# Performance work log

Hardware: AMD Instinct MI355X
Metric: run time of the kernel (lower is better)

The kernel has to match this reference:

```python
import jax, jax.numpy as jnp
import numpy as np

N, NUM_MEM, HIDDEN = 131072, 1024, 256
TEMPERATURE = 0.5
EPS = 1e-12  # matches F.normalize default eps


def setup_inputs() -> dict:
    key = jax.random.key(0)
    k1, k2 = jax.random.split(key)
    x = jax.random.normal(k1, (N, HIDDEN), dtype=jnp.float32)
    # xavier_uniform-style init for the memory bank
    limit = float(np.sqrt(6.0 / (NUM_MEM + HIDDEN)))
    memories = jax.random.uniform(k2, (NUM_MEM, HIDDEN), dtype=jnp.float32,
                                  minval=-limit, maxval=limit)
    return {"x": x, "memories": memories}


def reference(x, memories):
    # cosine similarity: normalize both sides, then QK^T
    x_norm = x / jnp.maximum(jnp.linalg.norm(x, axis=-1, keepdims=True), EPS)
    mem_norm = memories / jnp.maximum(
        jnp.linalg.norm(memories, axis=-1, keepdims=True), EPS)
    logits = jnp.einsum('nd,md->nm', x_norm, mem_norm) / TEMPERATURE
    weight = jax.nn.softmax(logits, axis=-1)        # [N, num_memories]
    read = jnp.einsum('nm,md->nd', weight, memories)  # weighted memory read
    return read
```

## Files before the change

### kernel.cpp

```cpp
#include <hip/hip_runtime.h>
#include <hip/hip_bf16.h>
#include <stdint.h>

#define HIDDEN 256
#define NMEM   1024
#define NTILES 32
#define LOG2E  1.44269504088896340736f

typedef __attribute__((ext_vector_type(8)))  short bf16x8;
typedef __attribute__((ext_vector_type(16))) float f32x16;
typedef unsigned short ushort_t;
typedef unsigned int   uint_t;

__device__ __forceinline__ ushort_t f2bf(float f) {
  uint_t u = __builtin_bit_cast(uint_t, f);
  u += 0x7FFFu + ((u >> 16) & 1u);
  return (ushort_t)(u >> 16);
}

__device__ __forceinline__ void gload_lds16(const void* g, void* l) {
  __builtin_amdgcn_global_load_lds(
      (const __attribute__((address_space(1))) uint_t*)g,
      (__attribute__((address_space(3))) uint_t*)l, 16, 0, 0);
}

__global__ void prep_kernel(const float* __restrict__ mem,
                            ushort_t* __restrict__ wsm,
                            ushort_t* __restrict__ wsv) {
  const int m = blockIdx.x;
  const int k = threadIdx.x;
  float v = mem[m * HIDDEN + k];
  float ss = v * v;
  #pragma unroll
  for (int off = 1; off < 64; off <<= 1) ss += __shfl_xor(ss, off);
  __shared__ float red[4];
  if ((k & 63) == 0) red[k >> 6] = ss;
  __syncthreads();
  const float tot = red[0] + red[1] + red[2] + red[3];
  const float inv = 1.0f / fmaxf(sqrtf(tot), 1e-12f);
  const ushort_t hn = f2bf(v * inv);
  const ushort_t hv = f2bf(v);
  const int t = m >> 5, mr = m & 31;
  wsm[t * 8192 + mr * 256 + (((k >> 3) ^ (mr & 7)) << 3) + (k & 7)] = hn;
  wsv[t * 8192 + k * 32  + (((mr >> 3) ^ ((k >> 1) & 3)) << 3) + (mr & 7)] = hv;
}

__global__ __launch_bounds__(256, 2) void mem_kernel(
    const float* __restrict__ x, const ushort_t* __restrict__ wsm,
    const ushort_t* __restrict__ wsv, float* __restrict__ out) {
  __shared__ __align__(16) char lds[65536];
  const int tid  = threadIdx.x;
  const int lane = tid & 63;
  const int wave = tid >> 6;
  const int col  = lane & 31;
  const int hi   = lane >> 5;
  const int row0 = blockIdx.x * 128 + wave * 32;
  const char* gm = (const char*)wsm;
  const char* gv = (const char*)wsv;

  auto stage = [&](int t, int buf) {
    const int bb = buf << 15;
    const int go = t * 16384;
    #pragma unroll
    for (int r = 0; r < 4; ++r) {
      const int o = wave * 4096 + r * 1024;
      gload_lds16(gm + go + o + lane * 16, lds + bb + o);
      gload_lds16(gv + go + o + lane * 16, lds + bb + 16384 + o);
    }
  };

  stage(0, 0);

  bf16x8 xb[16];
  float ss = 0.f;
  const float* xr = x + (size_t)(row0 + col) * HIDDEN + hi * 8;
  #pragma unroll
  for (int ks = 0; ks < 16; ++ks) {
    float4 a = *(const float4*)(xr + ks * 16);
    float4 b = *(const float4*)(xr + ks * 16 + 4);
    ss += a.x*a.x + a.y*a.y + a.z*a.z + a.w*a.w
        + b.x*b.x + b.y*b.y + b.z*b.z + b.w*b.w;
    xb[ks][0] = (short)f2bf(a.x); xb[ks][1] = (short)f2bf(a.y);
    xb[ks][2] = (short)f2bf(a.z); xb[ks][3] = (short)f2bf(a.w);
    xb[ks][4] = (short)f2bf(b.x); xb[ks][5] = (short)f2bf(b.y);
    xb[ks][6] = (short)f2bf(b.z); xb[ks][7] = (short)f2bf(b.w);
  }
  ss += __shfl_xor(ss, 32);
  const float myscale = (2.0f * LOG2E) / fmaxf(sqrtf(ss), 1e-12f);

  const f32x16 zz = {0.f,0.f,0.f,0.f, 0.f,0.f,0.f,0.f,
                     0.f,0.f,0.f,0.f, 0.f,0.f,0.f,0.f};
  f32x16 o8[8];
  #pragma unroll
  for (int i = 0; i < 8; ++i) o8[i] = zz;
  float den = 0.f;

  const int ck7 = col & 7;
  const int ck3 = (col >> 1) & 3;

  __syncthreads();

  for (int t = 0; t < NTILES; ++t) {
    const int mb = (t & 1) << 15;
    const int vb = mb + 16384;
    if (t < NTILES - 1) stage(t + 1, (t & 1) ^ 1);
    __builtin_amdgcn_s_setprio(1);

    const char* ab = lds + mb + col * 512;
    f32x16 s0 = zz, s1 = zz;
    #pragma unroll
    for (int ks2 = 0; ks2 < 8; ++ks2) {
      bf16x8 a0 = *(const bf16x8*)(ab + (((4*ks2 + hi)     ^ ck7) << 4));
      bf16x8 a1 = *(const bf16x8*)(ab + (((4*ks2 + 2 + hi) ^ ck7) << 4));
      s0 = __builtin_amdgcn_mfma_f32_32x32x16_bf16(a0, xb[2*ks2],   s0, 0,0,0);
      s1 = __builtin_amdgcn_mfma_f32_32x32x16_bf16(a1, xb[2*ks2+1], s1, 0,0,0);
    }

    float p[16];
    #pragma unroll
    for (int r = 0; r < 16; ++r) {
      const float pv = exp2f((s0[r] + s1[r]) * myscale);
      den += pv;
      p[r] = pv;
    }

    bf16x8 pa[2];
    #pragma unroll
    for (int ks = 0; ks < 2; ++ks) {
      const int b0 = ks * 8;
      uint_t w0 = (uint_t)f2bf(p[b0+0]) | ((uint_t)f2bf(p[b0+1]) << 16);
      uint_t w1 = (uint_t)f2bf(p[b0+2]) | ((uint_t)f2bf(p[b0+3]) << 16);
      uint_t w2 = (uint_t)f2bf(p[b0+4]) | ((uint_t)f2bf(p[b0+5]) << 16);
      uint_t w3 = (uint_t)f2bf(p[b0+6]) | ((uint_t)f2bf(p[b0+7]) << 16);
      asm("v_permlane32_swap_b32 %0, %1" : "+v"(w0), "+v"(w2));
      asm("v_permlane32_swap_b32 %0, %1" : "+v"(w1), "+v"(w3));
      uint4 u = {w0, w1, w2, w3};
      pa[ks] = __builtin_bit_cast(bf16x8, u);
    }

    const char* vrb = lds + vb + col * 64;
    #pragma unroll
    for (int ks = 0; ks < 2; ++ks) {
      const int cc = ((2*ks + hi) ^ ck3) << 4;
      #pragma unroll
      for (int d0 = 0; d0 < 8; ++d0) {
        bf16x8 vf = *(const bf16x8*)(vrb + d0 * 2048 + cc);
        o8[d0] = __builtin_amdgcn_mfma_f32_32x32x16_bf16(pa[ks], vf, o8[d0], 0,0,0);
      }
    }
    __builtin_amdgcn_s_setprio(0);
    __syncthreads();
  }

  den += __shfl_xor(den, 32);
  const float rden = 1.0f / den;
  float rdv[16];
  #pragma unroll
  for (int r = 0; r < 16; ++r)
    rdv[r] = __shfl(rden, (r & 3) + 8 * (r >> 2) + 4 * hi);

  float* op = out + (size_t)row0 * HIDDEN;
  #pragma unroll
  for (int d0 = 0; d0 < 8; ++d0) {
    #pragma unroll
    for (int r = 0; r < 16; ++r) {
      const int rw = (r & 3) + 8 * (r >> 2) + 4 * hi;
      op[(size_t)rw * HIDDEN + d0 * 32 + col] = o8[d0][r] * rdv[r];
    }
  }
}

extern "C" void kernel_launch(void* const* d_in, const int* in_sizes, int n_in,
                              void* d_out, int out_size, void* d_ws, size_t ws_size,
                              hipStream_t stream) {
  const float* x   = (const float*)d_in[0];
  const float* mem = (const float*)d_in[1];
  float* out = (float*)d_out;
  const int N = in_sizes[0] / HIDDEN;

  ushort_t* wsm = (ushort_t*)d_ws;
  ushort_t* wsv = wsm + NMEM * HIDDEN;

  prep_kernel<<<NMEM, HIDDEN, 0, stream>>>(mem, wsm, wsv);
  mem_kernel<<<N / 128, 256, 0, stream>>>(x, wsm, wsv, out);
}
```

Measured before the change: 371.7 us.

## Relayout LDS tiles for lane-linear reads and unroll double-buffer loop by two

Changes the prep kernel's global layout of the normalized and raw memory tiles so that each lane reads LDS at lane*16 plus compile-time offsets, removing the XOR swizzle address math. The tile loop is unrolled by two so buffer offsets become immediates. Softmax conversion now uses packed v_cvt_pk_bf16_f32 instead of manual rounding, with a tree-summed denominator. Priority is dropped around the exp section. The new lane-contiguous layout could change LDS bank conflict behaviour.

Result: faster. 347.2 us (-6.6%).

```diff
diff --git a/kernel.cpp b/kernel.cpp
--- a/kernel.cpp
+++ b/kernel.cpp
@@ -4,7 +4,6 @@
 
 #define HIDDEN 256
 #define NMEM   1024
-#define NTILES 32
 #define LOG2E  1.44269504088896340736f
 
 typedef __attribute__((ext_vector_type(8)))  short bf16x8;
@@ -41,8 +40,11 @@
   const ushort_t hn = f2bf(v * inv);
   const ushort_t hv = f2bf(v);
   const int t = m >> 5, mr = m & 31;
-  wsm[t * 8192 + mr * 256 + (((k >> 3) ^ (mr & 7)) << 3) + (k & 7)] = hn;
-  wsv[t * 8192 + k * 32  + (((mr >> 3) ^ ((k >> 1) & 3)) << 3) + (mr & 7)] = hv;
+  const int c = k >> 3;
+  wsm[t * 8192 + ((c >> 1) & 1) * 4096 + (c >> 2) * 512 + (c & 1) * 256
+      + mr * 8 + (k & 7)] = hn;
+  wsv[t * 8192 + (k >> 5) * 1024 + ((mr >> 3) >> 1) * 512 + ((mr >> 3) & 1) * 256
+      + (k & 31) * 8 + (mr & 7)] = hv;
 }
 
 __global__ __launch_bounds__(256, 2) void mem_kernel(
@@ -95,62 +97,70 @@
   for (int i = 0; i < 8; ++i) o8[i] = zz;
   float den = 0.f;
 
-  const int ck7 = col & 7;
-  const int ck3 = (col >> 1) & 3;
+  const char* ldsb = lds + lane * 16;
 
   __syncthreads();
 
-  for (int t = 0; t < NTILES; ++t) {
-    const int mb = (t & 1) << 15;
-    const int vb = mb + 16384;
-    if (t < NTILES - 1) stage(t + 1, (t & 1) ^ 1);
-    __builtin_amdgcn_s_setprio(1);
+#define TILE_BODY(IMM)                                                        \
+  do {                                                                        \
+    __builtin_amdgcn_s_setprio(1);                                            \
+    f32x16 s0 = zz, s1 = zz;                                                  \
+    _Pragma("unroll")                                                         \
+    for (int ks2 = 0; ks2 < 8; ++ks2) {                                       \
+      bf16x8 a0 = *(const bf16x8*)(ldsb + (IMM) + ks2 * 1024);                \
+      bf16x8 a1 = *(const bf16x8*)(ldsb + (IMM) + 8192 + ks2 * 1024);         \
+      s0 = __builtin_amdgcn_mfma_f32_32x32x16_bf16(a0, xb[2*ks2],   s0,0,0,0);\
+      s1 = __builtin_amdgcn_mfma_f32_32x32x16_bf16(a1, xb[2*ks2+1], s1,0,0,0);\
+    }                                                                         \
+    __builtin_amdgcn_s_setprio(0);                                            \
+    bf16x8 pa[2];                                                             \
+    _Pragma("unroll")                                                         \
+    for (int ks = 0; ks < 2; ++ks) {                                          \
+      const int b0 = ks * 8;                                                  \
+      const float e0 = exp2f((s0[b0+0] + s1[b0+0]) * myscale);                \
+      const float e1 = exp2f((s0[b0+1] + s1[b0+1]) * myscale);                \
+      const float e2 = exp2f((s0[b0+2] + s1[b0+2]) * myscale);                \
+      const float e3 = exp2f((s0[b0+3] + s1[b0+3]) * myscale);                \
+      const float e4 = exp2f((s0[b0+4] + s1[b0+4]) * myscale);                \
+      const float e5 = exp2f((s0[b0+5] + s1[b0+5]) * myscale);                \
+      const float e6 = exp2f((s0[b0+6] + s1[b0+6]) * myscale);                \
+      const float e7 = exp2f((s0[b0+7] + s1[b0+7]) * myscale);                \
+      den += ((e0 + e1) + (e2 + e3)) + ((e4 + e5) + (e6 + e7));               \
+      uint_t w0, w1, w2, w3;                                                  \
+      asm("v_cvt_pk_bf16_f32 %0, %1, %2" : "=v"(w0) : "v"(e0), "v"(e1));      \
+      asm("v_cvt_pk_bf16_f32 %0, %1, %2" : "=v"(w1) : "v"(e2), "v"(e3));      \
+      asm("v_cvt_pk_bf16_f32 %0, %1, %2" : "=v"(w2) : "v"(e4), "v"(e5));      \
+      asm("v_cvt_pk_bf16_f32 %0, %1, %2" : "=v"(w3) : "v"(e6), "v"(e7));      \
+      asm("v_permlane32_swap_b32 %0, %1" : "+v"(w0), "+v"(w2));               \
+      asm("v_permlane32_swap_b32 %0, %1" : "+v"(w1), "+v"(w3));               \
+      uint4 u = {w0, w1, w2, w3};                                             \
+      pa[ks] = __builtin_bit_cast(bf16x8, u);                                 \
+    }                                                                         \
+    __builtin_amdgcn_s_setprio(1);                                            \
+    _Pragma("unroll")                                                         \
+    for (int ks = 0; ks < 2; ++ks) {                                          \
+      _Pragma("unroll")                                                       \
+      for (int d0 = 0; d0 < 8; ++d0) {                                        \
+        bf16x8 vf = *(const bf16x8*)(ldsb + (IMM) + 16384 + ks * 1024         \
+                                     + d0 * 2048);                            \
+        o8[d0] = __builtin_amdgcn_mfma_f32_32x32x16_bf16(pa[ks], vf,          \
+                                                         o8[d0], 0,0,0);      \
+      }                                                                       \
+    }                                                                         \
+    __builtin_amdgcn_s_setprio(0);                                            \
+  } while (0)
 
-    const char* ab = lds + mb + col * 512;
-    f32x16 s0 = zz, s1 = zz;
-    #pragma unroll
-    for (int ks2 = 0; ks2 < 8; ++ks2) {
-      bf16x8 a0 = *(const bf16x8*)(ab + (((4*ks2 + hi)     ^ ck7) << 4));
-      bf16x8 a1 = *(const bf16x8*)(ab + (((4*ks2 + 2 + hi) ^ ck7) << 4));
-      s0 = __builtin_amdgcn_mfma_f32_32x32x16_bf16(a0, xb[2*ks2],   s0, 0,0,0);
-      s1 = __builtin_amdgcn_mfma_f32_32x32x16_bf16(a1, xb[2*ks2+1], s1, 0,0,0);
-    }
-
-    float p[16];
-    #pragma unroll
-    for (int r = 0; r < 16; ++r) {
-      const float pv = exp2f((s0[r] + s1[r]) * myscale);
-      den += pv;
-      p[r] = pv;
-    }
-
-    bf16x8 pa[2];
-    #pragma unroll
-    for (int ks = 0; ks < 2; ++ks) {
-      const int b0 = ks * 8;
-      uint_t w0 = (uint_t)f2bf(p[b0+0]) | ((uint_t)f2bf(p[b0+1]) << 16);
-      uint_t w1 = (uint_t)f2bf(p[b0+2]) | ((uint_t)f2bf(p[b0+3]) << 16);
-      uint_t w2 = (uint_t)f2bf(p[b0+4]) | ((uint_t)f2bf(p[b0+5]) << 16);
-      uint_t w3 = (uint_t)f2bf(p[b0+6]) | ((uint_t)f2bf(p[b0+7]) << 16);
-      asm("v_permlane32_swap_b32 %0, %1" : "+v"(w0), "+v"(w2));
-      asm("v_permlane32_swap_b32 %0, %1" : "+v"(w1), "+v"(w3));
-      uint4 u = {w0, w1, w2, w3};
-      pa[ks] = __builtin_bit_cast(bf16x8, u);
-    }
-
-    const char* vrb = lds + vb + col * 64;
-    #pragma unroll
-    for (int ks = 0; ks < 2; ++ks) {
-      const int cc = ((2*ks + hi) ^ ck3) << 4;
-      #pragma unroll
-      for (int d0 = 0; d0 < 8; ++d0) {
-        bf16x8 vf = *(const bf16x8*)(vrb + d0 * 2048 + cc);
-        o8[d0] = __builtin_amdgcn_mfma_f32_32x32x16_bf16(pa[ks], vf, o8[d0], 0,0,0);
-      }
-    }
-    __builtin_amdgcn_s_setprio(0);
+  #pragma unroll 1
+  for (int tt = 0; tt < 16; ++tt) {
+    const int te = tt * 2;
+    stage(te + 1, 1);
+    TILE_BODY(0);
+    __syncthreads();
+    if (te + 1 < 31) stage(te + 2, 0);
+    TILE_BODY(32768);
     __syncthreads();
   }
+#undef TILE_BODY
 
   den += __shfl_xor(den, 32);
   const float rden = 1.0f / den;
```
